# Performance work log

Measured on AMD Instinct MI355X. Metric: run time of the kernel, lower is better.

Reference implementation:

```python
import jax, jax.numpy as jnp
import numpy as np

EMBED_DIM = 1024
N_HEADS = 16
HEAD_DIM = EMBED_DIM // N_HEADS

def setup_inputs() -> dict:
    key = jax.random.key(0)
    kx, kq, kk, kv, ko = jax.random.split(key, 5)
    s = 1.0 / np.sqrt(EMBED_DIM)
    return {
        "x": jax.random.normal(kx, (4, 2048, EMBED_DIM), dtype=jnp.float32),
        "Wq": jax.random.normal(kq, (EMBED_DIM, EMBED_DIM), dtype=jnp.float32) * s,
        "Wk": jax.random.normal(kk, (EMBED_DIM, EMBED_DIM), dtype=jnp.float32) * s,
        "Wv": jax.random.normal(kv, (EMBED_DIM, EMBED_DIM), dtype=jnp.float32) * s,
        "Wo": jax.random.normal(ko, (EMBED_DIM, EMBED_DIM), dtype=jnp.float32) * s,
    }

def reference(x, Wq, Wk, Wv, Wo):
    B, T, D = x.shape
    H, Dh = N_HEADS, HEAD_DIM
    # projections (nn.Linear: y = x @ W.T); split heads -> [B, H, T, Dh]
    Q = (x @ Wq.T).reshape(B, T, H, Dh).transpose(0, 2, 1, 3)
    K = (x @ Wk.T).reshape(B, T, H, Dh).transpose(0, 2, 1, 3)
    V = (x @ Wv.T).reshape(B, T, H, Dh).transpose(0, 2, 1, 3)
    scores = jnp.einsum("bhqd,bhkd->bhqk", Q, K) / jnp.sqrt(jnp.float32(Dh))
    attn = jax.nn.softmax(scores, axis=-1)
    out = jnp.einsum("bhqk,bhkd->bhqd", attn, V)  # [B,H,T,Dh]
    out = out.transpose(0, 2, 1, 3).reshape(B, T, D)
    return out @ Wo.T
```

## Files before the change

kernel.cpp:

```cpp
#include <hip/hip_runtime.h>

typedef _Float16 f16;
typedef _Float16 f16x8 __attribute__((ext_vector_type(8)));
typedef _Float16 f16x4 __attribute__((ext_vector_type(4)));
typedef __fp16 h16x2 __attribute__((ext_vector_type(2)));
typedef float f32x4 __attribute__((ext_vector_type(4)));

#define MFMA16(a, b, c) __builtin_amdgcn_mfma_f32_16x16x32_f16((a), (b), (c), 0, 0, 0)
#define MEMBAR() __asm__ __volatile__("" ::: "memory")

__device__ __forceinline__ void cp16(const f16* g, f16* l) {
  __builtin_amdgcn_global_load_lds(
      (const __attribute__((address_space(1))) void*)g,
      (__attribute__((address_space(3))) void*)l, 16, 0, 0);
}

__global__ __launch_bounds__(256) void cvt_all(
    const float* __restrict__ x,  const float* __restrict__ Wq,
    const float* __restrict__ Wk, const float* __restrict__ Wv,
    const float* __restrict__ Wo,
    f16* __restrict__ X16, f16* __restrict__ Wq16, f16* __restrict__ Wk16,
    f16* __restrict__ Wv16, f16* __restrict__ Wo16) {
  int blk = blockIdx.x;
  const float* src; f16* dst; size_t off;
  if (blk < 4096) { src = x; dst = X16; off = (size_t)blk * 2048; }
  else {
    int t = blk - 4096, widx = t >> 9, loc = t & 511;
    src = (widx == 0) ? Wq : (widx == 1) ? Wk : (widx == 2) ? Wv : Wo;
    dst = (widx == 0) ? Wq16 : (widx == 1) ? Wk16 : (widx == 2) ? Wv16 : Wo16;
    off = (size_t)loc * 2048;
  }
  size_t e = off + (size_t)threadIdx.x * 8;
  const float4* s = (const float4*)(src + e);
  float4 a = s[0], b = s[1];
  f16x8 o;
  o[0] = (f16)a.x; o[1] = (f16)a.y; o[2] = (f16)a.z; o[3] = (f16)a.w;
  o[4] = (f16)b.x; o[5] = (f16)b.y; o[6] = (f16)b.z; o[7] = (f16)b.w;
  *(f16x8*)(dst + e) = o;
}

__device__ __forceinline__ void gemm_core(
    const f16* __restrict__ A, const f16* __restrict__ B, void* __restrict__ Cv,
    bool outF16, bool permT, int N, int K, int bm, int bn, float scale,
    f16* As, f16* Bs) {
  const int tid = threadIdx.x;
  const int lane = tid & 63, w = tid >> 6;
  const int wm = w >> 2, wn = w & 3;
  const int c = lane & 15, q = lane >> 4;
  const int key = (c >> 1) & 3;
  f32x4 acc[4][2] = {};

  const int Lrow = lane >> 2, Lp = (lane & 3) ^ ((lane >> 3) & 3);
  auto stage = [&](int k0, int bufi) {
    int r0 = w * 16;
    cp16(A + (size_t)(bm + r0 + Lrow) * K + k0 + Lp * 8,
         As + bufi * 4096 + r0 * 32 + lane * 8);
    cp16(B + (size_t)(bn + r0 + Lrow) * K + k0 + Lp * 8,
         Bs + bufi * 4096 + r0 * 32 + lane * 8);
  };

  const int NIT = K >> 5;
  stage(0, 0);
  stage(32, 1);
  for (int i = 0; i < NIT; ++i) {
    if (i + 1 < NIT) __builtin_amdgcn_s_waitcnt(0x0F72);
    else             __builtin_amdgcn_s_waitcnt(0x0F70);
    __builtin_amdgcn_s_barrier();
    MEMBAR();
    if (i + 2 < NIT) stage((i + 2) << 5, (i + 2) % 3);

    const f16* Ab = As + (i % 3) * 4096;
    const f16* Bb = Bs + (i % 3) * 4096;
    f16x8 af[4], bf[2];
#pragma unroll
    for (int mt = 0; mt < 4; ++mt)
      af[mt] = *(const f16x8*)(Ab + (wm * 64 + mt * 16 + c) * 32 + (q ^ key) * 8);
#pragma unroll
    for (int nt = 0; nt < 2; ++nt)
      bf[nt] = *(const f16x8*)(Bb + (wn * 32 + nt * 16 + c) * 32 + (q ^ key) * 8);
#pragma unroll
    for (int mt = 0; mt < 4; ++mt)
#pragma unroll
      for (int nt = 0; nt < 2; ++nt)
        acc[mt][nt] = MFMA16(af[mt], bf[nt], acc[mt][nt]);
    MEMBAR();
  }

#pragma unroll
  for (int mt = 0; mt < 4; ++mt)
#pragma unroll
    for (int nt = 0; nt < 2; ++nt)
#pragma unroll
      for (int r = 0; r < 4; ++r) {
        size_t row = bm + wm * 64 + mt * 16 + q * 4 + r;
        size_t col = bn + wn * 32 + nt * 16 + c;
        if (permT) {
          int t = (int)col & 63;
          col = (col & ~(size_t)63) |
                (size_t)((t & 0x23) | ((t & 0x0C) << 1) | ((t & 0x10) >> 2));
        }
        float v = acc[mt][nt][r] * scale;
        if (outF16) ((f16*)Cv)[row * N + col] = (f16)v;
        else ((float*)Cv)[row * N + col] = v;
      }
}

__global__ __launch_bounds__(512, 6) void gemm_qkvt(
    const f16* __restrict__ X, const f16* __restrict__ Wq,
    const f16* __restrict__ Wk, const f16* __restrict__ Wv,
    f16* __restrict__ Q, f16* __restrict__ Ko, f16* __restrict__ VT, float cs) {
  __shared__ __align__(16) f16 As[12288], Bs[12288];
  const int z = blockIdx.z, x = blockIdx.x;
  if (z < 2) {
    int bm = (x & 7) * 8 + (x >> 6), bn = (x >> 3) & 7;
    gemm_core(X, z ? Wk : Wq, z ? (void*)Ko : (void*)Q, true, false, 1024, 1024,
              bm * 128, bn * 128, z ? 1.0f : cs, As, Bs);
  } else {
    int bn = (x & 7) * 8 + ((x >> 3) & 7), bm = x >> 6;
    gemm_core(Wv, X, (void*)VT, true, true, 8192, 1024,
              bm * 128, bn * 128, 1.0f, As, Bs);
  }
}

__global__ __launch_bounds__(512, 6) void gemm_o(
    const f16* __restrict__ A, const f16* __restrict__ Wo, float* __restrict__ out) {
  __shared__ __align__(16) f16 As[12288], Bs[12288];
  const int x = blockIdx.x;
  int bm = (x & 7) * 8 + (x >> 6), bn = (x >> 3) & 7;
  gemm_core(A, Wo, (void*)out, false, false, 1024, 1024,
            bm * 128, bn * 128, 1.0f, As, Bs);
}

__global__ __launch_bounds__(256, 2) void attn_kernel(
    const f16* __restrict__ Qg, const f16* __restrict__ Kg,
    const f16* __restrict__ VTg, f16* __restrict__ Og) {
  const int T = 2048, D = 1024;
  const int x = blockIdx.x;
  const int xcd = x & 7, rem = x >> 3;
  const int qt = rem & 7, grp = rem >> 3;
  const int bh = (grp << 3) | xcd;
  const int b = bh >> 4, h = bh & 15;
  const size_t base = ((size_t)b * T) * D + h * 64;
  const size_t baseV = (size_t)h * 64 * 8192 + (size_t)b * T;
  __shared__ __align__(16) f16 smem[24576];
  const int tid = threadIdx.x;
  const int lane = tid & 63, w = tid >> 6;
  const int c = lane & 15, q = lane >> 4;
  const int cx = c & 7;
  f16* Kb = smem;
  f16* Vb = smem + 12288;

#pragma unroll
  for (int j = 0; j < 8; ++j) {
    int cb = (w * 8 + j) * 64;
    int ch = cb + lane;
    int row = ch >> 3, p = (ch & 7) ^ (row & 7);
    cp16(Qg + base + (size_t)(qt * 256 + row) * D + p * 8, smem + cb * 8);
  }
  __syncthreads();
  f16x8 qf[4][2];
#pragma unroll
  for (int g = 0; g < 4; ++g)
#pragma unroll
    for (int kh = 0; kh < 2; ++kh)
      qf[g][kh] = *(const f16x8*)(smem + (w * 64 + g * 16 + c) * 64 + ((kh * 4 + q) ^ cx) * 8);
  __syncthreads();

  f32x4 o_[4][4] = {};
  f32x4 acc_l[4] = {};
  const f32x4 zero4 = {0.f, 0.f, 0.f, 0.f};
  f16x8 onesf;
#pragma unroll
  for (int j = 0; j < 8; ++j) onesf[j] = (f16)1.0f;

  union U8 { f16x8 v; h16x2 h[4]; };

  auto stageKV = [&](int kv, int bufi) {
    f16* Ks = Kb + bufi * 4096;
    f16* Vt = Vb + bufi * 4096;
#pragma unroll
    for (int j = 0; j < 2; ++j) {
      int cb = (w * 2 + j) * 64;
      int ch = cb + lane;
      int row = ch >> 3, p = (ch & 7) ^ (row & 7);
      cp16(Kg + base + (size_t)(kv + row) * D + p * 8, Ks + cb * 8);
    }
#pragma unroll
    for (int j = 0; j < 2; ++j) {
      int cb = (w * 2 + j) * 64;
      int ch = cb + lane;
      int row = ch >> 3, p = (ch & 7) ^ (row & 7);
      cp16(VTg + baseV + (size_t)row * 8192 + kv + p * 8, Vt + cb * 8);
    }
  };

  auto loadKF = [&](const f16* Ks, f16x8 kf[2][4]) {
#pragma unroll
    for (int kh = 0; kh < 2; ++kh)
#pragma unroll
      for (int mt = 0; mt < 4; ++mt)
        kf[kh][mt] = *(const f16x8*)(Ks + (mt * 16 + c) * 64 + ((kh * 4 + q) ^ cx) * 8);
  };

  f32x4 st[4][4];

  stageKV(0, 0);
  stageKV(64, 1);
  __builtin_amdgcn_s_waitcnt(0x0F74);
  __builtin_amdgcn_s_barrier();
  MEMBAR();
  {
    f16x8 kf[2][4];
    loadKF(Kb, kf);
    __builtin_amdgcn_s_setprio(1);
#pragma unroll
    for (int mt = 0; mt < 4; ++mt)
#pragma unroll
      for (int g = 0; g < 4; ++g)
        st[mt][g] = MFMA16(kf[0][mt], qf[g][0], zero4);
#pragma unroll
    for (int mt = 0; mt < 4; ++mt)
#pragma unroll
      for (int g = 0; g < 4; ++g)
        st[mt][g] = MFMA16(kf[1][mt], qf[g][1], st[mt][g]);
    __builtin_amdgcn_s_setprio(0);
  }

  for (int i = 0; i < 31; ++i) {
    __builtin_amdgcn_s_waitcnt(0x0F70);
    __builtin_amdgcn_s_barrier();
    MEMBAR();
    if (i < 30) stageKV((i + 2) * 64, (i + 2) % 3);

    f16x8 kf[2][4];
    loadKF(Kb + ((i + 1) % 3) * 4096, kf);

    U8 pf[4][2];
#pragma unroll
    for (int g = 0; g < 4; ++g)
#pragma unroll
      for (int mt = 0; mt < 4; ++mt) {
        float p0 = __builtin_amdgcn_exp2f(st[mt][g][0]);
        float p1 = __builtin_amdgcn_exp2f(st[mt][g][1]);
        float p2 = __builtin_amdgcn_exp2f(st[mt][g][2]);
        float p3 = __builtin_amdgcn_exp2f(st[mt][g][3]);
        pf[g][mt >> 1].h[(mt & 1) * 2 + 0] = __builtin_amdgcn_cvt_pkrtz(p0, p1);
        pf[g][mt >> 1].h[(mt & 1) * 2 + 1] = __builtin_amdgcn_cvt_pkrtz(p2, p3);
      }

    __builtin_amdgcn_s_setprio(1);
#pragma unroll
    for (int mt = 0; mt < 4; ++mt)
#pragma unroll
      for (int g = 0; g < 4; ++g)
        st[mt][g] = MFMA16(kf[0][mt], qf[g][0], zero4);
#pragma unroll
    for (int mt = 0; mt < 4; ++mt)
#pragma unroll
      for (int g = 0; g < 4; ++g)
        st[mt][g] = MFMA16(kf[1][mt], qf[g][1], st[mt][g]);

    const f16* Vt = Vb + (i % 3) * 4096;
#pragma unroll
    for (int kc = 0; kc < 2; ++kc) {
#pragma unroll
      for (int d = 0; d < 4; ++d) {
        f16x8 vf = *(const f16x8*)(Vt + (d * 16 + c) * 64 + ((kc * 4 + q) ^ cx) * 8);
        o_[0][d] = MFMA16(pf[0][kc].v, vf, o_[0][d]);
        o_[1][d] = MFMA16(pf[1][kc].v, vf, o_[1][d]);
        o_[2][d] = MFMA16(pf[2][kc].v, vf, o_[2][d]);
        o_[3][d] = MFMA16(pf[3][kc].v, vf, o_[3][d]);
      }
      acc_l[0] = MFMA16(pf[0][kc].v, onesf, acc_l[0]);
      acc_l[1] = MFMA16(pf[1][kc].v, onesf, acc_l[1]);
      acc_l[2] = MFMA16(pf[2][kc].v, onesf, acc_l[2]);
      acc_l[3] = MFMA16(pf[3][kc].v, onesf, acc_l[3]);
    }
    __builtin_amdgcn_s_setprio(0);
    MEMBAR();
  }

  {
    U8 pf[4][2];
#pragma unroll
    for (int g = 0; g < 4; ++g)
#pragma unroll
      for (int mt = 0; mt < 4; ++mt) {
        float p0 = __builtin_amdgcn_exp2f(st[mt][g][0]);
        float p1 = __builtin_amdgcn_exp2f(st[mt][g][1]);
        float p2 = __builtin_amdgcn_exp2f(st[mt][g][2]);
        float p3 = __builtin_amdgcn_exp2f(st[mt][g][3]);
        pf[g][mt >> 1].h[(mt & 1) * 2 + 0] = __builtin_amdgcn_cvt_pkrtz(p0, p1);
        pf[g][mt >> 1].h[(mt & 1) * 2 + 1] = __builtin_amdgcn_cvt_pkrtz(p2, p3);
      }
    const f16* Vt = Vb + (31 % 3) * 4096;
    __builtin_amdgcn_s_setprio(1);
#pragma unroll
    for (int kc = 0; kc < 2; ++kc) {
#pragma unroll
      for (int d = 0; d < 4; ++d) {
        f16x8 vf = *(const f16x8*)(Vt + (d * 16 + c) * 64 + ((kc * 4 + q) ^ cx) * 8);
        o_[0][d] = MFMA16(pf[0][kc].v, vf, o_[0][d]);
        o_[1][d] = MFMA16(pf[1][kc].v, vf, o_[1][d]);
        o_[2][d] = MFMA16(pf[2][kc].v, vf, o_[2][d]);
        o_[3][d] = MFMA16(pf[3][kc].v, vf, o_[3][d]);
      }
      acc_l[0] = MFMA16(pf[0][kc].v, onesf, acc_l[0]);
      acc_l[1] = MFMA16(pf[1][kc].v, onesf, acc_l[1]);
      acc_l[2] = MFMA16(pf[2][kc].v, onesf, acc_l[2]);
      acc_l[3] = MFMA16(pf[3][kc].v, onesf, acc_l[3]);
    }
    __builtin_amdgcn_s_setprio(0);
  }

#pragma unroll
  for (int g = 0; g < 4; ++g)
#pragma unroll
    for (int r = 0; r < 4; ++r) {
      float linv = 1.0f / acc_l[g][r];
      size_t row = (size_t)qt * 256 + w * 64 + g * 16 + q * 4 + r;
#pragma unroll
      for (int d = 0; d < 4; ++d)
        Og[base + row * D + d * 16 + c] = (f16)(o_[g][d][r] * linv);
    }
}

extern "C" void kernel_launch(void* const* d_in, const int* in_sizes, int n_in,
                              void* d_out, int out_size, void* d_ws, size_t ws_size,
                              hipStream_t stream) {
  const float* x  = (const float*)d_in[0];
  const float* Wq = (const float*)d_in[1];
  const float* Wk = (const float*)d_in[2];
  const float* Wv = (const float*)d_in[3];
  const float* Wo = (const float*)d_in[4];
  char* ws = (char*)d_ws;
  const size_t MB = 1ull << 20;
  f16* X16  = (f16*)(ws + 0 * MB);
  f16* Wq16 = (f16*)(ws + 16 * MB);
  f16* Wk16 = (f16*)(ws + 18 * MB);
  f16* Wv16 = (f16*)(ws + 20 * MB);
  f16* Wo16 = (f16*)(ws + 22 * MB);
  f16* Q16  = (f16*)(ws + 24 * MB);
  f16* K16  = (f16*)(ws + 40 * MB);
  f16* VT16 = (f16*)(ws + 56 * MB);
  f16* A16  = (f16*)(ws + 72 * MB);

  const float cs = 0.18033688011112042f;

  cvt_all<<<6144, 256, 0, stream>>>(x, Wq, Wk, Wv, Wo,
                                    X16, Wq16, Wk16, Wv16, Wo16);

  gemm_qkvt<<<dim3(512, 1, 3), 512, 0, stream>>>(
      X16, Wq16, Wk16, Wv16, Q16, K16, VT16, cs);

  attn_kernel<<<dim3(512, 1, 1), 256, 0, stream>>>(Q16, K16, VT16, A16);

  gemm_o<<<512, 512, 0, stream>>>(A16, Wo16, (float*)d_out);
}
```

Baseline: 260.1 us.

## Fuse Q and K projections sharing X tiles; compute softmax row sums with VALU

The Q and K projection GEMMs are merged into one block that loads each X tile once and multiplies it against both Wq and Wk tiles, using a three-buffer shared-memory pipeline. The grid shrinks from three z-slices to two, and occupancy hints drop to match the larger shared-memory footprint. In attention, the extra MFMAs against a ones vector that computed softmax denominators are replaced with scalar adds plus lane shuffles at the end. This trades MFMA work for VALU adds and changes occupancy and register pressure in the projection kernel.

Measured after the change: 246.7 us. 1.05x faster.

```diff
diff --git a/kernel.cpp b/kernel.cpp
--- a/kernel.cpp
+++ b/kernel.cpp
@@ -105,21 +105,84 @@
       }
 }
 
-__global__ __launch_bounds__(512, 6) void gemm_qkvt(
+__global__ __launch_bounds__(512, 4) void gemm_qkvt(
     const f16* __restrict__ X, const f16* __restrict__ Wq,
     const f16* __restrict__ Wk, const f16* __restrict__ Wv,
     f16* __restrict__ Q, f16* __restrict__ Ko, f16* __restrict__ VT, float cs) {
-  __shared__ __align__(16) f16 As[12288], Bs[12288];
+  __shared__ __align__(16) f16 smem[36864];
   const int z = blockIdx.z, x = blockIdx.x;
-  if (z < 2) {
-    int bm = (x & 7) * 8 + (x >> 6), bn = (x >> 3) & 7;
-    gemm_core(X, z ? Wk : Wq, z ? (void*)Ko : (void*)Q, true, false, 1024, 1024,
-              bm * 128, bn * 128, z ? 1.0f : cs, As, Bs);
-  } else {
+  if (z == 1) {
     int bn = (x & 7) * 8 + ((x >> 3) & 7), bm = x >> 6;
     gemm_core(Wv, X, (void*)VT, true, true, 8192, 1024,
-              bm * 128, bn * 128, 1.0f, As, Bs);
-  }
+              bm * 128, bn * 128, 1.0f, smem, smem + 12288);
+    return;
+  }
+  const int bm = ((x & 7) * 8 + (x >> 6)) * 128;
+  const int bn = ((x >> 3) & 7) * 128;
+  f16* Xs = smem;
+  f16* Qs = smem + 12288;
+  f16* Ks = smem + 24576;
+  const int tid = threadIdx.x;
+  const int lane = tid & 63, w = tid >> 6;
+  const int wm = w >> 2, wn = w & 3;
+  const int c = lane & 15, q = lane >> 4;
+  const int key = (c >> 1) & 3;
+  f32x4 accq[4][2] = {}, acck[4][2] = {};
+
+  const int Lrow = lane >> 2, Lp = (lane & 3) ^ ((lane >> 3) & 3);
+  auto stage = [&](int k0, int bufi) {
+    int r0 = w * 16;
+    cp16(X  + (size_t)(bm + r0 + Lrow) * 1024 + k0 + Lp * 8,
+         Xs + bufi * 4096 + r0 * 32 + lane * 8);
+    cp16(Wq + (size_t)(bn + r0 + Lrow) * 1024 + k0 + Lp * 8,
+         Qs + bufi * 4096 + r0 * 32 + lane * 8);
+    cp16(Wk + (size_t)(bn + r0 + Lrow) * 1024 + k0 + Lp * 8,
+         Ks + bufi * 4096 + r0 * 32 + lane * 8);
+  };
+
+  const int NIT = 32;
+  stage(0, 0);
+  stage(32, 1);
+  for (int i = 0; i < NIT; ++i) {
+    if (i + 1 < NIT) __builtin_amdgcn_s_waitcnt(0x0F73);
+    else             __builtin_amdgcn_s_waitcnt(0x0F70);
+    __builtin_amdgcn_s_barrier();
+    MEMBAR();
+    if (i + 2 < NIT) stage((i + 2) << 5, (i + 2) % 3);
+
+    const f16* Xb = Xs + (i % 3) * 4096;
+    const f16* Qb = Qs + (i % 3) * 4096;
+    const f16* Kb2 = Ks + (i % 3) * 4096;
+    f16x8 af[4], bq[2], bk[2];
+#pragma unroll
+    for (int mt = 0; mt < 4; ++mt)
+      af[mt] = *(const f16x8*)(Xb + (wm * 64 + mt * 16 + c) * 32 + (q ^ key) * 8);
+#pragma unroll
+    for (int nt = 0; nt < 2; ++nt) {
+      bq[nt] = *(const f16x8*)(Qb + (wn * 32 + nt * 16 + c) * 32 + (q ^ key) * 8);
+      bk[nt] = *(const f16x8*)(Kb2 + (wn * 32 + nt * 16 + c) * 32 + (q ^ key) * 8);
+    }
+#pragma unroll
+    for (int mt = 0; mt < 4; ++mt)
+#pragma unroll
+      for (int nt = 0; nt < 2; ++nt) {
+        accq[mt][nt] = MFMA16(af[mt], bq[nt], accq[mt][nt]);
+        acck[mt][nt] = MFMA16(af[mt], bk[nt], acck[mt][nt]);
+      }
+    MEMBAR();
+  }
+
+#pragma unroll
+  for (int mt = 0; mt < 4; ++mt)
+#pragma unroll
+    for (int nt = 0; nt < 2; ++nt)
+#pragma unroll
+      for (int r = 0; r < 4; ++r) {
+        size_t row = bm + wm * 64 + mt * 16 + q * 4 + r;
+        size_t col = bn + wn * 32 + nt * 16 + c;
+        Q[row * 1024 + col]  = (f16)(accq[mt][nt][r] * cs);
+        Ko[row * 1024 + col] = (f16)acck[mt][nt][r];
+      }
 }
 
 __global__ __launch_bounds__(512, 6) void gemm_o(
@@ -166,13 +229,9 @@
       qf[g][kh] = *(const f16x8*)(smem + (w * 64 + g * 16 + c) * 64 + ((kh * 4 + q) ^ cx) * 8);
   __syncthreads();
 
+  float l_[4] = {0.f, 0.f, 0.f, 0.f};
   f32x4 o_[4][4] = {};
-  f32x4 acc_l[4] = {};
   const f32x4 zero4 = {0.f, 0.f, 0.f, 0.f};
-  f16x8 onesf;
-#pragma unroll
-  for (int j = 0; j < 8; ++j) onesf[j] = (f16)1.0f;
-
   union U8 { f16x8 v; h16x2 h[4]; };
 
   auto stageKV = [&](int kv, int bufi) {
@@ -237,16 +296,20 @@
 
     U8 pf[4][2];
 #pragma unroll
-    for (int g = 0; g < 4; ++g)
+    for (int g = 0; g < 4; ++g) {
+      float s = 0.f;
 #pragma unroll
       for (int mt = 0; mt < 4; ++mt) {
         float p0 = __builtin_amdgcn_exp2f(st[mt][g][0]);
         float p1 = __builtin_amdgcn_exp2f(st[mt][g][1]);
         float p2 = __builtin_amdgcn_exp2f(st[mt][g][2]);
         float p3 = __builtin_amdgcn_exp2f(st[mt][g][3]);
+        s += (p0 + p1) + (p2 + p3);
         pf[g][mt >> 1].h[(mt & 1) * 2 + 0] = __builtin_amdgcn_cvt_pkrtz(p0, p1);
         pf[g][mt >> 1].h[(mt & 1) * 2 + 1] = __builtin_amdgcn_cvt_pkrtz(p2, p3);
       }
+      l_[g] += s;
+    }
 
     __builtin_amdgcn_s_setprio(1);
 #pragma unroll
@@ -262,7 +325,7 @@
 
     const f16* Vt = Vb + (i % 3) * 4096;
 #pragma unroll
-    for (int kc = 0; kc < 2; ++kc) {
+    for (int kc = 0; kc < 2; ++kc)
 #pragma unroll
       for (int d = 0; d < 4; ++d) {
         f16x8 vf = *(const f16x8*)(Vt + (d * 16 + c) * 64 + ((kc * 4 + q) ^ cx) * 8);
@@ -271,11 +334,6 @@
         o_[2][d] = MFMA16(pf[2][kc].v, vf, o_[2][d]);
         o_[3][d] = MFMA16(pf[3][kc].v, vf, o_[3][d]);
       }
-      acc_l[0] = MFMA16(pf[0][kc].v, onesf, acc_l[0]);
-      acc_l[1] = MFMA16(pf[1][kc].v, onesf, acc_l[1]);
-      acc_l[2] = MFMA16(pf[2][kc].v, onesf, acc_l[2]);
-      acc_l[3] = MFMA16(pf[3][kc].v, onesf, acc_l[3]);
-    }
     __builtin_amdgcn_s_setprio(0);
     MEMBAR();
   }
@@ -283,20 +341,24 @@
   {
     U8 pf[4][2];
 #pragma unroll
-    for (int g = 0; g < 4; ++g)
+    for (int g = 0; g < 4; ++g) {
+      float s = 0.f;
 #pragma unroll
       for (int mt = 0; mt < 4; ++mt) {
         float p0 = __builtin_amdgcn_exp2f(st[mt][g][0]);
         float p1 = __builtin_amdgcn_exp2f(st[mt][g][1]);
         float p2 = __builtin_amdgcn_exp2f(st[mt][g][2]);
         float p3 = __builtin_amdgcn_exp2f(st[mt][g][3]);
+        s += (p0 + p1) + (p2 + p3);
         pf[g][mt >> 1].h[(mt & 1) * 2 + 0] = __builtin_amdgcn_cvt_pkrtz(p0, p1);
         pf[g][mt >> 1].h[(mt & 1) * 2 + 1] = __builtin_amdgcn_cvt_pkrtz(p2, p3);
       }
+      l_[g] += s;
+    }
     const f16* Vt = Vb + (31 % 3) * 4096;
     __builtin_amdgcn_s_setprio(1);
 #pragma unroll
-    for (int kc = 0; kc < 2; ++kc) {
+    for (int kc = 0; kc < 2; ++kc)
 #pragma unroll
       for (int d = 0; d < 4; ++d) {
         f16x8 vf = *(const f16x8*)(Vt + (d * 16 + c) * 64 + ((kc * 4 + q) ^ cx) * 8);
@@ -305,19 +367,20 @@
         o_[2][d] = MFMA16(pf[2][kc].v, vf, o_[2][d]);
         o_[3][d] = MFMA16(pf[3][kc].v, vf, o_[3][d]);
       }
-      acc_l[0] = MFMA16(pf[0][kc].v, onesf, acc_l[0]);
-      acc_l[1] = MFMA16(pf[1][kc].v, onesf, acc_l[1]);
-      acc_l[2] = MFMA16(pf[2][kc].v, onesf, acc_l[2]);
-      acc_l[3] = MFMA16(pf[3][kc].v, onesf, acc_l[3]);
-    }
     __builtin_amdgcn_s_setprio(0);
   }
 
 #pragma unroll
+  for (int g = 0; g < 4; ++g) {
+    l_[g] += __shfl_xor(l_[g], 16);
+    l_[g] += __shfl_xor(l_[g], 32);
+  }
+
+#pragma unroll
   for (int g = 0; g < 4; ++g)
 #pragma unroll
     for (int r = 0; r < 4; ++r) {
-      float linv = 1.0f / acc_l[g][r];
+      float linv = 1.0f / __shfl(l_[g], q * 4 + r);
       size_t row = (size_t)qt * 256 + w * 64 + g * 16 + q * 4 + r;
 #pragma unroll
       for (int d = 0; d < 4; ++d)
@@ -350,7 +413,7 @@
   cvt_all<<<6144, 256, 0, stream>>>(x, Wq, Wk, Wv, Wo,
                                     X16, Wq16, Wk16, Wv16, Wo16);
 
-  gemm_qkvt<<<dim3(512, 1, 3), 512, 0, stream>>>(
+  gemm_qkvt<<<dim3(512, 1, 2), 512, 0, stream>>>(
       X16, Wq16, Wk16, Wv16, Q16, K16, VT16, cs);
 
   attn_kernel<<<dim3(512, 1, 1), 256, 0, stream>>>(Q16, K16, VT16, A16);
```
